# Kernel tuning notes

Measured on AMD Instinct MI355X. Metric: run time of the kernel, lower is better.

The kernel has to match this reference:

```python
import jax, jax.numpy as jnp
import numpy as np

B, P, ENC = 32, 196, 2048   # batch, num_pixels, encoder_dim
A, D, E = 512, 512, 512     # attention_dim, decoder_dim, embed_dim
V, L = 32000, 40            # vocab_size, caption length
T = L - 1                   # max decode steps (static)


def setup_inputs() -> dict:
    key = jax.random.key(0)
    ks = jax.random.split(key, 20)
    u = lambda k, shape, s=0.05: jax.random.uniform(k, shape, jnp.float32, -s, s)
    caplens = jax.random.randint(ks[2], (B,), 5, L + 1).at[0].set(L)
    return {
        "encoder_out": jax.random.normal(ks[0], (B, P, ENC), jnp.float32),
        "encoded_captions": jax.random.randint(ks[1], (B, L), 0, V),
        "caption_lengths": caplens,
        "embedding": u(ks[3], (V, E), 0.1),
        "W_enc": u(ks[4], (ENC, A)), "b_enc": jnp.zeros((A,), jnp.float32),
        "W_dec": u(ks[5], (D, A)),   "b_dec": jnp.zeros((A,), jnp.float32),
        "w_att": u(ks[6], (A, 1)),   "b_att": jnp.zeros((1,), jnp.float32),
        "W_ih": u(ks[7], (E + ENC, 4 * D)), "b_ih": jnp.zeros((4 * D,), jnp.float32),
        "W_hh": u(ks[8], (D, 4 * D)),       "b_hh": jnp.zeros((4 * D,), jnp.float32),
        "W_h": u(ks[9], (ENC, D)),  "b_h": jnp.zeros((D,), jnp.float32),
        "W_c": u(ks[10], (ENC, D)), "b_c": jnp.zeros((D,), jnp.float32),
        "W_fb": u(ks[11], (D, ENC)), "b_fb": jnp.zeros((ENC,), jnp.float32),
        "W_fc": u(ks[12], (D, V), 0.1), "b_fc": jnp.zeros((V,), jnp.float32),
    }


def reference(encoder_out, encoded_captions, caption_lengths, embedding,
              W_enc, b_enc, W_dec, b_dec, w_att, b_att,
              W_ih, b_ih, W_hh, b_hh, W_h, b_h, W_c, b_c,
              W_fb, b_fb, W_fc, b_fc):
    dec_len = caption_lengths - 1                       # [B]
    embs = embedding[encoded_captions]                  # [B, L, E]
    avg = encoder_out.mean(axis=1)                      # [B, ENC]
    h0 = avg @ W_h + b_h                                # [B, D]
    c0 = avg @ W_c + b_c
    enc_att = encoder_out @ W_enc + b_enc               # [B, P, A] (loop-invariant)

    xs = (jnp.transpose(embs[:, :T], (1, 0, 2)), jnp.arange(T))

    def step(carry, xt):
        h, c = carry
        emb_t, t = xt                                   # [B, E], scalar
        active = dec_len > t                            # [B] bool
        dec = h @ W_dec + b_dec                         # [B, A]
        e = (jax.nn.relu(enc_att + dec[:, None, :]) @ w_att)[..., 0] + b_att[0]  # [B, P]
        alpha = jax.nn.softmax(e, axis=1)               # [B, P]
        awe = jnp.einsum('bp,bpd->bd', alpha, encoder_out)
        gate = jax.nn.sigmoid(h @ W_fb + b_fb)          # [B, ENC]
        awe = gate * awe
        x = jnp.concatenate([emb_t, awe], axis=-1)      # [B, E+ENC]
        g = x @ W_ih + b_ih + h @ W_hh + b_hh           # [B, 4D]
        i_, f_, g_, o_ = jnp.split(g, 4, axis=-1)
        c_new = jax.nn.sigmoid(f_) * c + jax.nn.sigmoid(i_) * jnp.tanh(g_)
        h_new = jax.nn.sigmoid(o_) * jnp.tanh(c_new)
        preds = h_new @ W_fc + b_fc                     # [B, V]
        m = active[:, None].astype(h.dtype)
        h = jnp.where(active[:, None], h_new, h)        # only active rows advance
        c = jnp.where(active[:, None], c_new, c)
        return (h, c), (preds * m, alpha * m)

    (_, _), (preds, alphas) = jax.lax.scan(step, (h0, c0), xs)
    predictions = jnp.transpose(preds, (1, 0, 2))       # [B, T, V]
    alphas = jnp.transpose(alphas, (1, 0, 2))           # [B, T, P]
    return predictions, alphas
```

## Files before the change

### kernel.cpp

```cpp
#include <hip/hip_runtime.h>
#include <math.h>

#define NB 32
#define NP 196
#define ENC 2048
#define VOC 32000
#define LCAP 40
#define TS 39

typedef unsigned int uint_t;
typedef unsigned short ushort_t;

__device__ __forceinline__ float sigm(float x) { return 1.f / (1.f + expf(-x)); }

__device__ __forceinline__ ushort_t f2bf(float f) {
  uint_t u = __float_as_uint(f);
  u = (u + 0x7FFFu + ((u >> 16) & 1u)) >> 16;
  return (ushort_t)u;
}
__device__ __forceinline__ float bf2f(ushort_t s) { return __uint_as_float(((uint_t)s) << 16); }

typedef __attribute__((ext_vector_type(8))) short bf8v;
typedef __attribute__((ext_vector_type(16))) float f16v;
typedef __attribute__((ext_vector_type(4))) float f4v;

__device__ __forceinline__ f16v MFMA(bf8v a, bf8v b, f16v c) {
  return __builtin_amdgcn_mfma_f32_32x32x16_bf16(a, b, c, 0, 0, 0);
}

__device__ __forceinline__ void mfma_pipe_frag(
    const ushort_t* __restrict__ pa_h, const ushort_t* __restrict__ pa_l,
    const ushort_t* __restrict__ pb_h, const ushort_t* __restrict__ pb_l,
    int nquad, f16v& acc)
{
  bf8v ah0 = *(const bf8v*)(pa_h +    0), al0 = *(const bf8v*)(pa_l +    0);
  bf8v bh0 = *(const bf8v*)(pb_h +    0), bl0 = *(const bf8v*)(pb_l +    0);
  bf8v ah1 = *(const bf8v*)(pa_h +  512), al1 = *(const bf8v*)(pa_l +  512);
  bf8v bh1 = *(const bf8v*)(pb_h +  512), bl1 = *(const bf8v*)(pb_l +  512);
  bf8v ah2 = *(const bf8v*)(pa_h + 1024), al2 = *(const bf8v*)(pa_l + 1024);
  bf8v bh2 = *(const bf8v*)(pb_h + 1024), bl2 = *(const bf8v*)(pb_l + 1024);
  bf8v ah3 = *(const bf8v*)(pa_h + 1536), al3 = *(const bf8v*)(pa_l + 1536);
  bf8v bh3 = *(const bf8v*)(pb_h + 1536), bl3 = *(const bf8v*)(pb_l + 1536);
  for (int q = 0; q < nquad; ++q) {
    const size_t nk = (size_t)(q + 1) * 2048;
    const bool more = (q + 1 < nquad);
    acc = MFMA(ah0, bh0, acc); acc = MFMA(ah0, bl0, acc); acc = MFMA(al0, bh0, acc);
    if (more) {
      ah0 = *(const bf8v*)(pa_h + nk +    0); al0 = *(const bf8v*)(pa_l + nk +    0);
      bh0 = *(const bf8v*)(pb_h + nk +    0); bl0 = *(const bf8v*)(pb_l + nk +    0);
    }
    acc = MFMA(ah1, bh1, acc); acc = MFMA(ah1, bl1, acc); acc = MFMA(al1, bh1, acc);
    if (more) {
      ah1 = *(const bf8v*)(pa_h + nk +  512); al1 = *(const bf8v*)(pa_l + nk +  512);
      bh1 = *(const bf8v*)(pb_h + nk +  512); bl1 = *(const bf8v*)(pb_l + nk +  512);
    }
    acc = MFMA(ah2, bh2, acc); acc = MFMA(ah2, bl2, acc); acc = MFMA(al2, bh2, acc);
    if (more) {
      ah2 = *(const bf8v*)(pa_h + nk + 1024); al2 = *(const bf8v*)(pa_l + nk + 1024);
      bh2 = *(const bf8v*)(pb_h + nk + 1024); bl2 = *(const bf8v*)(pb_l + nk + 1024);
    }
    acc = MFMA(ah3, bh3, acc); acc = MFMA(ah3, bl3, acc); acc = MFMA(al3, bh3, acc);
    if (more) {
      ah3 = *(const bf8v*)(pa_h + nk + 1536); al3 = *(const bf8v*)(pa_l + nk + 1536);
      bh3 = *(const bf8v*)(pb_h + nk + 1536); bl3 = *(const bf8v*)(pb_l + nk + 1536);
    }
  }
}

__device__ __forceinline__ void mfma_pipe_fragAH(
    const ushort_t* __restrict__ pa_h,
    const ushort_t* __restrict__ pb_h, const ushort_t* __restrict__ pb_l,
    int nquad, f16v& acc)
{
  bf8v ah0 = *(const bf8v*)(pa_h +    0);
  bf8v bh0 = *(const bf8v*)(pb_h +    0), bl0 = *(const bf8v*)(pb_l +    0);
  bf8v ah1 = *(const bf8v*)(pa_h +  512);
  bf8v bh1 = *(const bf8v*)(pb_h +  512), bl1 = *(const bf8v*)(pb_l +  512);
  bf8v ah2 = *(const bf8v*)(pa_h + 1024);
  bf8v bh2 = *(const bf8v*)(pb_h + 1024), bl2 = *(const bf8v*)(pb_l + 1024);
  bf8v ah3 = *(const bf8v*)(pa_h + 1536);
  bf8v bh3 = *(const bf8v*)(pb_h + 1536), bl3 = *(const bf8v*)(pb_l + 1536);
  for (int q = 0; q < nquad; ++q) {
    const size_t nk = (size_t)(q + 1) * 2048;
    const bool more = (q + 1 < nquad);
    acc = MFMA(ah0, bh0, acc); acc = MFMA(ah0, bl0, acc);
    if (more) {
      ah0 = *(const bf8v*)(pa_h + nk +    0);
      bh0 = *(const bf8v*)(pb_h + nk +    0); bl0 = *(const bf8v*)(pb_l + nk +    0);
    }
    acc = MFMA(ah1, bh1, acc); acc = MFMA(ah1, bl1, acc);
    if (more) {
      ah1 = *(const bf8v*)(pa_h + nk +  512);
      bh1 = *(const bf8v*)(pb_h + nk +  512); bl1 = *(const bf8v*)(pb_l + nk +  512);
    }
    acc = MFMA(ah2, bh2, acc); acc = MFMA(ah2, bl2, acc);
    if (more) {
      ah2 = *(const bf8v*)(pa_h + nk + 1024);
      bh2 = *(const bf8v*)(pb_h + nk + 1024); bl2 = *(const bf8v*)(pb_l + nk + 1024);
    }
    acc = MFMA(ah3, bh3, acc); acc = MFMA(ah3, bl3, acc);
    if (more) {
      ah3 = *(const bf8v*)(pa_h + nk + 1536);
      bh3 = *(const bf8v*)(pb_h + nk + 1536); bl3 = *(const bf8v*)(pb_l + nk + 1536);
    }
  }
}

__device__ __forceinline__ void mfma_pipe_fragHH(
    const ushort_t* __restrict__ pa_h,
    const ushort_t* __restrict__ pb_h, int nquad, f16v& acc)
{
  bf8v ah0 = *(const bf8v*)(pa_h +    0);
  bf8v bh0 = *(const bf8v*)(pb_h +    0);
  bf8v ah1 = *(const bf8v*)(pa_h +  512);
  bf8v bh1 = *(const bf8v*)(pb_h +  512);
  bf8v ah2 = *(const bf8v*)(pa_h + 1024);
  bf8v bh2 = *(const bf8v*)(pb_h + 1024);
  bf8v ah3 = *(const bf8v*)(pa_h + 1536);
  bf8v bh3 = *(const bf8v*)(pb_h + 1536);
  for (int q = 0; q < nquad; ++q) {
    const size_t nk = (size_t)(q + 1) * 2048;
    const bool more = (q + 1 < nquad);
    acc = MFMA(ah0, bh0, acc);
    if (more) { ah0 = *(const bf8v*)(pa_h + nk +    0); bh0 = *(const bf8v*)(pb_h + nk +    0); }
    acc = MFMA(ah1, bh1, acc);
    if (more) { ah1 = *(const bf8v*)(pa_h + nk +  512); bh1 = *(const bf8v*)(pb_h + nk +  512); }
    acc = MFMA(ah2, bh2, acc);
    if (more) { ah2 = *(const bf8v*)(pa_h + nk + 1024); bh2 = *(const bf8v*)(pb_h + nk + 1024); }
    acc = MFMA(ah3, bh3, acc);
    if (more) { ah3 = *(const bf8v*)(pa_h + nk + 1536); bh3 = *(const bf8v*)(pb_h + nk + 1536); }
  }
}

#define CD_ROW(rr, g) (((rr) & 3) + 8 * ((rr) >> 2) + 4 * (g))

__global__ __launch_bounds__(256) void menc_att(
    const ushort_t* __restrict__ Ahi,
    const ushort_t* __restrict__ Whi, const ushort_t* __restrict__ Wlo,
    const float* __restrict__ benc, ushort_t* __restrict__ encatt_bf)
{
  __shared__ float tileS[4][32][33];
  int w = threadIdx.x >> 6, lane = threadIdx.x & 63;
  int mt = blockIdx.y;
  int ct = blockIdx.x * 4 + w;
  const ushort_t* pa_h = Ahi + ((size_t)mt * 128) * 512 + lane * 8;
  const ushort_t* pb_h = Whi + ((size_t)ct * 128) * 512 + lane * 8;
  const ushort_t* pb_l = Wlo + ((size_t)ct * 128) * 512 + lane * 8;
  f16v acc = (f16v)(0.0f);
  mfma_pipe_fragAH(pa_h, pb_h, pb_l, 32, acc);
  int r = lane & 31, g = lane >> 5;
  float bn = benc[ct * 32 + r];
#pragma unroll
  for (int rr = 0; rr < 16; ++rr)
    tileS[w][r][CD_ROW(rr, g)] = acc[rr] + bn;
  __syncthreads();
#pragma unroll
  for (int j = 0; j < 4; ++j) {
    int a_l = j * 8 + (lane >> 3);
    int p4 = (lane & 7) * 4;
    int n2 = ct * 32 + a_l;
#pragma unroll
    for (int jj = 0; jj < 4; ++jj) {
      int pl = p4 + jj;
      int rg = mt * 32 + pl;
      int b = rg / 196, pp = rg - b * 196;
      encatt_bf[((size_t)b * 512 + n2) * 196 + pp] = f2bf(tileS[w][a_l][pl]);
    }
  }
}

__global__ __launch_bounds__(256) void mk1(
    const ushort_t* __restrict__ hhi, const ushort_t* __restrict__ hlo,
    const ushort_t* __restrict__ W1hi, const ushort_t* __restrict__ W1lo,
    float* __restrict__ dec_gate)
{
  int w = threadIdx.x >> 6, lane = threadIdx.x & 63;
  int ct = blockIdx.x * 4 + w;
  const ushort_t* pa_h = hhi + lane * 8;
  const ushort_t* pa_l = hlo + lane * 8;
  const ushort_t* pb_h = W1hi + ((size_t)ct * 32) * 512 + lane * 8;
  const ushort_t* pb_l = W1lo + ((size_t)ct * 32) * 512 + lane * 8;
  f16v acc = (f16v)(0.0f);
  mfma_pipe_frag(pa_h, pa_l, pb_h, pb_l, 8, acc);
  int r = lane & 31, g = lane >> 5;
  int n = ct * 32 + r;
#pragma unroll
  for (int rr = 0; rr < 16; ++rr)
    dec_gate[CD_ROW(rr, g) * 2560 + n] = acc[rr];
}

__global__ __launch_bounds__(256) void mk3(
    const ushort_t* __restrict__ xhi, const ushort_t* __restrict__ xlo,
    const ushort_t* __restrict__ W3hi, const ushort_t* __restrict__ W3lo,
    float* __restrict__ P2)
{
  int w = threadIdx.x >> 6, lane = threadIdx.x & 63;
  int ct = blockIdx.x * 4 + w;
  int s = blockIdx.y;
  const ushort_t* pa_h = xhi + ((size_t)s * 20) * 512 + lane * 8;
  const ushort_t* pa_l = xlo + ((size_t)s * 20) * 512 + lane * 8;
  const ushort_t* pb_h = W3hi + ((size_t)ct * 160 + s * 20) * 512 + lane * 8;
  const ushort_t* pb_l = W3lo + ((size_t)ct * 160 + s * 20) * 512 + lane * 8;
  f16v acc = (f16v)(0.0f);
  mfma_pipe_frag(pa_h, pa_l, pb_h, pb_l, 5, acc);
  int r = lane & 31, g = lane >> 5;
  int n = ct * 32 + r;
#pragma unroll
  for (int rr = 0; rr < 16; ++rr)
    P2[(size_t)s * (32 * 2048) + CD_ROW(rr, g) * 2048 + n] = acc[rr];
}

__global__ __launch_bounds__(256) void mpreds(
    const ushort_t* __restrict__ hhist_hi,
    const ushort_t* __restrict__ Wfchi, const float* __restrict__ bfc,
    const int* __restrict__ clen, float* __restrict__ outp)
{
  int orig = blockIdx.x;
  int xcd = orig & 7, i = orig >> 3;
  int base = (xcd < 6) ? xcd * 1219 : 6 * 1219 + (xcd - 6) * 1218;
  int wgid = base + i;
  int ct4 = wgid / 39, mt = wgid - ct4 * 39;
  int w = threadIdx.x >> 6, lane = threadIdx.x & 63;
  int ct = ct4 * 4 + w;
  const ushort_t* pa_h = hhist_hi + ((size_t)mt * 32) * 512 + lane * 8;
  const ushort_t* pb_h = Wfchi + ((size_t)ct * 32) * 512 + lane * 8;
  f16v acc = (f16v)(0.0f);
  mfma_pipe_fragHH(pa_h, pb_h, 8, acc);
  int r = lane & 31, g = lane >> 5;
  int n = ct * 32 + r;
  float bn = bfc[n];
#pragma unroll
  for (int rr = 0; rr < 16; ++rr) {
    int b = CD_ROW(rr, g);
    bool act = clen[b] - 1 > mt;
    outp[(size_t)b * (TS * VOC) + (size_t)mt * VOC + n] = act ? (acc[rr] + bn) : 0.f;
  }
}

__global__ __launch_bounds__(256) void convAe_fused(
    const float* __restrict__ src, ushort_t* __restrict__ dhi,
    ushort_t* __restrict__ enc_bf)
{
  int mt = blockIdx.x;
  int kc = blockIdx.y * 4 + (threadIdx.x >> 6);
  int l = threadIdx.x & 63;
  int r = l & 31, g = l >> 5;
  size_t si = (size_t)(mt * 32 + r) * 2048 + kc * 16 + g * 8;
  const float* s = src + si;
  float4 v0 = *(const float4*)s, v1 = *(const float4*)(s + 4);
  ushort4 h0, h1;
  h0.x = f2bf(v0.x); h0.y = f2bf(v0.y); h0.z = f2bf(v0.z); h0.w = f2bf(v0.w);
  h1.x = f2bf(v1.x); h1.y = f2bf(v1.y); h1.z = f2bf(v1.z); h1.w = f2bf(v1.w);
  size_t off = ((size_t)mt * 128 + kc) * 512 + (size_t)l * 8;
  *(ushort4*)&dhi[off] = h0; *(ushort4*)&dhi[off + 4] = h1;
  *(ushort4*)&enc_bf[si] = h0; *(ushort4*)&enc_bf[si + 4] = h1;
}

__global__ __launch_bounds__(256) void convA_emb_frag(
    const float* __restrict__ Emb, const int* __restrict__ caps,
    ushort_t* __restrict__ dhi, ushort_t* __restrict__ dlo)
{
  int mt = blockIdx.x;
  int kc = blockIdx.y * 4 + (threadIdx.x >> 6);
  int l = threadIdx.x & 63;
  int r = l & 31, g = l >> 5;
  int tok = caps[r * LCAP + mt];
  const float* s = Emb + (size_t)tok * 512 + kc * 16 + g * 8;
  float4 v0 = *(const float4*)s, v1 = *(const float4*)(s + 4);
  ushort4 h0, l0, h1, l1;
  h0.x = f2bf(v0.x); l0.x = f2bf(v0.x - bf2f(h0.x));
  h0.y = f2bf(v0.y); l0.y = f2bf(v0.y - bf2f(h0.y));
  h0.z = f2bf(v0.z); l0.z = f2bf(v0.z - bf2f(h0.z));
  h0.w = f2bf(v0.w); l0.w = f2bf(v0.w - bf2f(h0.w));
  h1.x = f2bf(v1.x); l1.x = f2bf(v1.x - bf2f(h1.x));
  h1.y = f2bf(v1.y); l1.y = f2bf(v1.y - bf2f(h1.y));
  h1.z = f2bf(v1.z); l1.z = f2bf(v1.z - bf2f(h1.z));
  h1.w = f2bf(v1.w); l1.w = f2bf(v1.w - bf2f(h1.w));
  size_t off = ((size_t)mt * 32 + kc) * 512 + (size_t)l * 8;
  *(ushort4*)&dhi[off] = h0; *(ushort4*)&dhi[off + 4] = h1;
  *(ushort4*)&dlo[off] = l0; *(ushort4*)&dlo[off + 4] = l1;
}

__global__ __launch_bounds__(256) void convT_frag(
    const float* __restrict__ src, int N,
    ushort_t* __restrict__ dhi, ushort_t* __restrict__ dlo,
    int nkc_dst, int kc_off)
{
  int ct = blockIdx.x;
  int kc = blockIdx.y * 4 + (threadIdx.x >> 6);
  int l = threadIdx.x & 63;
  int c = l & 31, g = l >> 5;
  const float* s = src + (size_t)(kc * 16 + g * 8) * N + ct * 32 + c;
  ushort_t hi8[8], lo8[8];
#pragma unroll
  for (int e = 0; e < 8; ++e) {
    float f = s[(size_t)e * N];
    hi8[e] = f2bf(f); lo8[e] = f2bf(f - bf2f(hi8[e]));
  }
  size_t off = ((size_t)ct * nkc_dst + kc_off + kc) * 512 + (size_t)l * 8;
  *(ushort4*)&dhi[off]     = make_ushort4(hi8[0], hi8[1], hi8[2], hi8[3]);
  *(ushort4*)&dhi[off + 4] = make_ushort4(hi8[4], hi8[5], hi8[6], hi8[7]);
  *(ushort4*)&dlo[off]     = make_ushort4(lo8[0], lo8[1], lo8[2], lo8[3]);
  *(ushort4*)&dlo[off + 4] = make_ushort4(lo8[4], lo8[5], lo8[6], lo8[7]);
}

__global__ __launch_bounds__(256) void convT_fragH(
    const float* __restrict__ src, int N,
    ushort_t* __restrict__ dhi, int nkc_dst, int kc_off)
{
  int ct = blockIdx.x;
  int kc = blockIdx.y * 4 + (threadIdx.x >> 6);
  int l = threadIdx.x & 63;
  int c = l & 31, g = l >> 5;
  const float* s = src + (size_t)(kc * 16 + g * 8) * N + ct * 32 + c;
  ushort_t hi8[8];
#pragma unroll
  for (int e = 0; e < 8; ++e) hi8[e] = f2bf(s[(size_t)e * N]);
  size_t off = ((size_t)ct * nkc_dst + kc_off + kc) * 512 + (size_t)l * 8;
  *(ushort4*)&dhi[off]     = make_ushort4(hi8[0], hi8[1], hi8[2], hi8[3]);
  *(ushort4*)&dhi[off + 4] = make_ushort4(hi8[4], hi8[5], hi8[6], hi8[7]);
}

__global__ __launch_bounds__(256) void mavg_frag(
    const float* __restrict__ enc, ushort_t* __restrict__ dhi, ushort_t* __restrict__ dlo)
{
  int b = blockIdx.x;
  int e = blockIdx.y * 256 + threadIdx.x;
  float s = 0.f;
  const float* base = enc + (size_t)b * 196 * 2048 + e;
  for (int p = 0; p < NP; ++p) s += base[(size_t)p * 2048];
  s *= (1.f / 196.f);
  ushort_t hi = f2bf(s), lo = f2bf(s - bf2f(hi));
  size_t off = (size_t)(e >> 4) * 512 + ((e >> 3) & 1) * 256 + b * 8 + (e & 7);
  dhi[off] = hi; dlo[off] = lo;
}

__global__ __launch_bounds__(256) void mh0c0(
    const ushort_t* __restrict__ avg_hi, const ushort_t* __restrict__ avg_lo,
    const ushort_t* __restrict__ Whc_hi, const ushort_t* __restrict__ Whc_lo,
    const float* __restrict__ b_h, const float* __restrict__ b_c,
    float* __restrict__ h0f, float* __restrict__ cbuf)
{
  int w = threadIdx.x >> 6, lane = threadIdx.x & 63;
  int ct = blockIdx.x * 4 + w;
  const ushort_t* pa_h = avg_hi + lane * 8;
  const ushort_t* pa_l = avg_lo + lane * 8;
  const ushort_t* pb_h = Whc_hi + ((size_t)ct * 128) * 512 + lane * 8;
  const ushort_t* pb_l = Whc_lo + ((size_t)ct * 128) * 512 + lane * 8;
  f16v acc = (f16v)(0.0f);
  mfma_pipe_frag(pa_h, pa_l, pb_h, pb_l, 32, acc);
  int r = lane & 31, g = lane >> 5;
  int n = ct * 32 + r;
  if (ct < 16) {
    float bn = b_h[n];
#pragma unroll
    for (int rr = 0; rr < 16; ++rr)
      h0f[CD_ROW(rr, g) * 512 + n] = acc[rr] + bn;
  } else {
    int n2 = n - 512;
    float bn = b_c[n2];
#pragma unroll
    for (int rr = 0; rr < 16; ++rr)
      cbuf[CD_ROW(rr, g) * 512 + n2] = acc[rr] + bn;
  }
}

__global__ __launch_bounds__(256) void m_emb(
    const ushort_t* __restrict__ eFhi, const ushort_t* __restrict__ eFlo,
    const ushort_t* __restrict__ Whi, const ushort_t* __restrict__ Wlo,
    const float* __restrict__ b1, const float* __restrict__ b2,
    float* __restrict__ embproj)
{
  int w = threadIdx.x >> 6, lane = threadIdx.x & 63;
  int mt = blockIdx.y;
  int ct = blockIdx.x * 4 + w;
  const ushort_t* pa_h = eFhi + ((size_t)mt * 32) * 512 + lane * 8;
  const ushort_t* pa_l = eFlo + ((size_t)mt * 32) * 512 + lane * 8;
  const ushort_t* pb_h = Whi + ((size_t)ct * 32) * 512 + lane * 8;
  const ushort_t* pb_l = Wlo + ((size_t)ct * 32) * 512 + lane * 8;
  f16v acc = (f16v)(0.0f);
  mfma_pipe_frag(pa_h, pa_l, pb_h, pb_l, 8, acc);
  int r = lane & 31, g = lane >> 5;
  int n = ct * 32 + r;
  float bn = b1[n] + b2[n];
#pragma unroll
  for (int rr = 0; rr < 16; ++rr)
    embproj[(size_t)(mt * 32 + CD_ROW(rr, g)) * 2048 + n] = acc[rr] + bn;
}

__global__ __launch_bounds__(256) void hsplit_frag(
    const float* __restrict__ h0f,
    ushort_t* __restrict__ hhi, ushort_t* __restrict__ hlo,
    ushort_t* __restrict__ xhi, ushort_t* __restrict__ xlo)
{
  int idx = blockIdx.x * 256 + threadIdx.x;
  int b = idx >> 6, dq = idx & 63, d0 = dq << 3;
  ushort4 h0v, h1v, l0v, l1v;
  ushort_t hh[8], hl[8];
#pragma unroll
  for (int j = 0; j < 8; ++j) {
    float v = h0f[b * 512 + d0 + j];
    hh[j] = f2bf(v); hl[j] = f2bf(v - bf2f(hh[j]));
  }
  h0v = make_ushort4(hh[0], hh[1], hh[2], hh[3]); h1v = make_ushort4(hh[4], hh[5], hh[6], hh[7]);
  l0v = make_ushort4(hl[0], hl[1], hl[2], hl[3]); l1v = make_ushort4(hl[4], hl[5], hl[6], hl[7]);
  int kc = d0 >> 4, g = (d0 >> 3) & 1;
  size_t off = ((size_t)kc * 64 + g * 32 + b) * 8;
  *(ushort4*)&hhi[off] = h0v; *(ushort4*)&hhi[off + 4] = h1v;
  *(ushort4*)&hlo[off] = l0v; *(ushort4*)&hlo[off + 4] = l1v;
  int xk0 = 2048 + d0;
  size_t offx = ((size_t)(xk0 >> 4) * 64 + g * 32 + b) * 8;
  *(ushort4*)&xhi[offx] = h0v; *(ushort4*)&xhi[offx + 4] = h1v;
  *(ushort4*)&xlo[offx] = l0v; *(ushort4*)&xlo[offx + 4] = l1v;
}

__global__ __launch_bounds__(512) void k2ab(
    const float* __restrict__ dec_gate, const float* __restrict__ bdec,
    const float* __restrict__ bfb, const float* __restrict__ watt,
    const float* __restrict__ batt, const ushort_t* __restrict__ encatt_bf,
    const ushort_t* __restrict__ enc_bf, const int* __restrict__ clen,
    float* __restrict__ outa, ushort_t* __restrict__ xhi, ushort_t* __restrict__ xlo,
    int t)
{
  int b = blockIdx.x, yh = blockIdx.y, tid = threadIdx.x;
  __shared__ float dec_s[512], watt_s[512], part_s[2][256], red_s[256], al_s[196];
  __shared__ float aw_s[2][256][4];
  dec_s[tid] = dec_gate[b * 2560 + tid] + bdec[tid];
  watt_s[tid] = watt[tid];
  __syncthreads();
  int p = tid & 255, half = tid >> 8;
  float acc = 0.f;
  if (p < NP) {
    const ushort_t* col = encatt_bf + (size_t)b * 512 * 196 + p;
    int a0 = half * 256;
#pragma unroll 8
    for (int a = a0; a < a0 + 256; ++a)
      acc += fmaxf(bf2f(col[(size_t)a * 196]) + dec_s[a], 0.f) * watt_s[a];
  }
  part_s[half][p] = acc;
  __syncthreads();
  float e = -1e30f;
  if (tid < NP) e = part_s[0][tid] + part_s[1][tid] + batt[0];
  if (tid < 256) red_s[tid] = e;
  __syncthreads();
  for (int wd = 128; wd > 0; wd >>= 1) {
    if (tid < wd) red_s[tid] = fmaxf(red_s[tid], red_s[tid + wd]);
    __syncthreads();
  }
  float m = red_s[0];
  __syncthreads();
  float ex = (tid < NP) ? expf(e - m) : 0.f;
  if (tid < 256) red_s[tid] = ex;
  __syncthreads();
  for (int wd = 128; wd > 0; wd >>= 1) {
    if (tid < wd) red_s[tid] += red_s[tid + wd];
    __syncthreads();
  }
  float inv = 1.f / red_s[0];
  if (tid < NP) {
    float al = ex * inv;
    al_s[tid] = al;
    if (yh == 0) {
      bool act = clen[b] - 1 > t;
      outa[(size_t)(b * TS + t) * NP + tid] = act ? al : 0.f;
    }
  }
  __syncthreads();
  int q = tid & 255, sp = tid >> 8;
  int d = yh * 1024 + q * 4;
  float ax = 0.f, ay = 0.f, az = 0.f, aw = 0.f;
  int p0 = sp * 98;
#pragma unroll 7
  for (int pp = p0; pp < p0 + 98; ++pp) {
    float al = al_s[pp];
    ushort4 ev = *(const ushort4*)&enc_bf[(size_t)(b * NP + pp) * ENC + d];
    ax += al * bf2f(ev.x); ay += al * bf2f(ev.y);
    az += al * bf2f(ev.z); aw += al * bf2f(ev.w);
  }
  aw_s[sp][q][0] = ax; aw_s[sp][q][1] = ay; aw_s[sp][q][2] = az; aw_s[sp][q][3] = aw;
  __syncthreads();
  if (sp == 0) {
    ax += aw_s[1][q][0]; ay += aw_s[1][q][1];
    az += aw_s[1][q][2]; aw += aw_s[1][q][3];
    float4 gg = *(const float4*)&dec_gate[b * 2560 + 512 + d];
    float4 bb = *(const float4*)&bfb[d];
    float v0 = sigm(gg.x + bb.x) * ax;
    float v1 = sigm(gg.y + bb.y) * ay;
    float v2 = sigm(gg.z + bb.z) * az;
    float v3 = sigm(gg.w + bb.w) * aw;
    ushort4 hi, lo;
    hi.x = f2bf(v0); lo.x = f2bf(v0 - bf2f(hi.x));
    hi.y = f2bf(v1); lo.y = f2bf(v1 - bf2f(hi.y));
    hi.z = f2bf(v2); lo.z = f2bf(v2 - bf2f(hi.z));
    hi.w = f2bf(v3); lo.w = f2bf(v3 - bf2f(hi.w));
    size_t off = ((size_t)(d >> 4) * 64 + ((d >> 3) & 1) * 32 + b) * 8 + (d & 7);
    *(ushort4*)&xhi[off] = hi;
    *(ushort4*)&xlo[off] = lo;
  }
}

__global__ __launch_bounds__(64) void k4_lstm_frag(
    const float* __restrict__ P2, const float* __restrict__ embproj,
    const int* __restrict__ clen, float* __restrict__ c,
    ushort_t* __restrict__ hhi, ushort_t* __restrict__ hlo,
    ushort_t* __restrict__ xhi, ushort_t* __restrict__ xlo,
    ushort_t* __restrict__ hhist_hi, int t)
{
  int idx = blockIdx.x * 64 + threadIdx.x;
  int b = idx >> 6, dq = idx & 63, d0 = dq << 3;
  bool act = clen[b] - 1 > t;
  const float* ep = embproj + (size_t)(t * 32 + b) * 2048;
  f4v i0 = *(const f4v*)&ep[d0],        i1 = *(const f4v*)&ep[d0 + 4];
  f4v f0 = *(const f4v*)&ep[512 + d0],  f1 = *(const f4v*)&ep[512 + d0 + 4];
  f4v g0 = *(const f4v*)&ep[1024 + d0], g1 = *(const f4v*)&ep[1024 + d0 + 4];
  f4v o0 = *(const f4v*)&ep[1536 + d0], o1 = *(const f4v*)&ep[1536 + d0 + 4];
#pragma unroll
  for (int s = 0; s < 8; ++s) {
    const float* p2 = P2 + (size_t)s * 65536 + b * 2048;
    i0 += *(const f4v*)&p2[d0];        i1 += *(const f4v*)&p2[d0 + 4];
    f0 += *(const f4v*)&p2[512 + d0];  f1 += *(const f4v*)&p2[512 + d0 + 4];
    g0 += *(const f4v*)&p2[1024 + d0]; g1 += *(const f4v*)&p2[1024 + d0 + 4];
    o0 += *(const f4v*)&p2[1536 + d0]; o1 += *(const f4v*)&p2[1536 + d0 + 4];
  }
  f4v c0 = *(const f4v*)&c[b * 512 + d0], c1 = *(const f4v*)&c[b * 512 + d0 + 4];
  ushort_t hh[8], hl[8];
  f4v cn0, cn1;
#pragma unroll
  for (int j = 0; j < 8; ++j) {
    float iv = j < 4 ? i0[j] : i1[j - 4];
    float fv = j < 4 ? f0[j] : f1[j - 4];
    float gv = j < 4 ? g0[j] : g1[j - 4];
    float ov = j < 4 ? o0[j] : o1[j - 4];
    float cv = j < 4 ? c0[j] : c1[j - 4];
    float cn = sigm(fv) * cv + sigm(iv) * tanhf(gv);
    float hn = sigm(ov) * tanhf(cn);
    if (j < 4) cn0[j] = cn; else cn1[j - 4] = cn;
    hh[j] = f2bf(hn); hl[j] = f2bf(hn - bf2f(hh[j]));
  }
  ushort4 h0v = make_ushort4(hh[0], hh[1], hh[2], hh[3]);
  ushort4 h1v = make_ushort4(hh[4], hh[5], hh[6], hh[7]);
  ushort4 l0v = make_ushort4(hl[0], hl[1], hl[2], hl[3]);
  ushort4 l1v = make_ushort4(hl[4], hl[5], hl[6], hl[7]);
  int kc = d0 >> 4, g = (d0 >> 3) & 1;
  size_t offh = ((size_t)(t * 32 + kc)) * 512 + ((size_t)g * 32 + b) * 8;
  *(ushort4*)&hhist_hi[offh] = h0v; *(ushort4*)&hhist_hi[offh + 4] = h1v;
  if (!act) return;
  *(f4v*)&c[b * 512 + d0] = cn0; *(f4v*)&c[b * 512 + d0 + 4] = cn1;
  size_t off = ((size_t)kc * 64 + g * 32 + b) * 8;
  *(ushort4*)&hhi[off] = h0v; *(ushort4*)&hhi[off + 4] = h1v;
  *(ushort4*)&hlo[off] = l0v; *(ushort4*)&hlo[off + 4] = l1v;
  int xk0 = 2048 + d0;
  size_t offx = ((size_t)(xk0 >> 4) * 64 + g * 32 + b) * 8;
  *(ushort4*)&xhi[offx] = h0v; *(ushort4*)&xhi[offx + 4] = h1v;
  *(ushort4*)&xlo[offx] = l0v; *(ushort4*)&xlo[offx + 4] = l1v;
}

extern "C" void kernel_launch(void* const* d_in, const int* in_sizes, int n_in,
                              void* d_out, int out_size, void* d_ws, size_t ws_size,
                              hipStream_t stream)
{
  (void)in_sizes; (void)n_in; (void)out_size; (void)ws_size;
  const float* enc   = (const float*)d_in[0];
  const int*   caps  = (const int*)d_in[1];
  const int*   clen  = (const int*)d_in[2];
  const float* emb   = (const float*)d_in[3];
  const float* W_enc = (const float*)d_in[4];
  const float* b_enc = (const float*)d_in[5];
  const float* W_dec = (const float*)d_in[6];
  const float* b_dec = (const float*)d_in[7];
  const float* w_att = (const float*)d_in[8];
  const float* b_att = (const float*)d_in[9];
  const float* W_ih  = (const float*)d_in[10];
  const float* b_ih  = (const float*)d_in[11];
  const float* W_hh  = (const float*)d_in[12];
  const float* b_hh  = (const float*)d_in[13];
  const float* W_h   = (const float*)d_in[14];
  const float* b_h   = (const float*)d_in[15];
  const float* W_c   = (const float*)d_in[16];
  const float* b_c   = (const float*)d_in[17];
  const float* W_fb  = (const float*)d_in[18];
  const float* b_fb  = (const float*)d_in[19];
  const float* W_fc  = (const float*)d_in[20];
  const float* b_fc  = (const float*)d_in[21];

  float* out_preds = (float*)d_out;
  float* out_alpha = out_preds + (size_t)NB * TS * VOC;

  char* p = (char*)d_ws;
  ushort_t* encatt_bf = (ushort_t*)p;     p += 12845056;
  float* embproj  = (float*)p;            p += 10223616;
  float* P2buf    = (float*)p;            p += 2097152;
  float* dec_gate = (float*)p;            p += 327680;
  ushort_t* x_lo  = (ushort_t*)p;         p += 262144;
  float* h0f      = (float*)p;            p += 65536;
  float* cbuf     = (float*)p;            p += 65536;
  float* al_ws    = (float*)p;            p += 25088;
  ushort_t* h_hi  = (ushort_t*)p;         p += 32768;
  ushort_t* h_lo  = (ushort_t*)p;         p += 32768;
  ushort_t* x_hi  = (ushort_t*)p;         p += 163840;
  p += 262144 - 25088 - 32768 - 32768 - 163840;
  ushort_t* e_hi  = (ushort_t*)p;         p += 25690112;
  ushort_t* enc_bf = (ushort_t*)p;        p += 25690112;
  ushort_t* We_hi = (ushort_t*)p;         p += 2097152;
  ushort_t* We_lo = (ushort_t*)p;         p += 2097152;
  ushort_t* W1_hi = (ushort_t*)p;         p += 2621440;
  ushort_t* W1_lo = (ushort_t*)p;         p += 2621440;
  ushort_t* W3_hi = (ushort_t*)p;         p += 10485760;
  ushort_t* W3_lo = (ushort_t*)p;         p += 10485760;
  ushort_t* Wf_hi = (ushort_t*)p;         p += 32768000;
  ushort_t* WiE_hi = (ushort_t*)p;        p += 2097152;
  ushort_t* WiE_lo = (ushort_t*)p;        p += 2097152;
  ushort_t* eF_hi  = (ushort_t*)p;        p += 1277952;
  ushort_t* eF_lo  = (ushort_t*)p;        p += 1277952;
  ushort_t* hh_hi  = (ushort_t*)p;        p += 1277952;
  (void)al_ws;

  ushort_t* avg_hi = (ushort_t*)embproj;
  ushort_t* avg_lo = avg_hi + 65536;
  ushort_t* Whc_hi = Wf_hi;
  ushort_t* Whc_lo = Wf_hi + 2097152;

  mavg_frag<<<dim3(32, 8), 256, 0, stream>>>(enc, avg_hi, avg_lo);
  convT_frag<<<dim3(16, 32), 256, 0, stream>>>(W_h, 512, Whc_hi, Whc_lo, 128, 0);
  convT_frag<<<dim3(16, 32), 256, 0, stream>>>(W_c, 512,
      Whc_hi + (size_t)16 * 128 * 512, Whc_lo + (size_t)16 * 128 * 512, 128, 0);
  mh0c0<<<dim3(8), 256, 0, stream>>>(avg_hi, avg_lo, Whc_hi, Whc_lo, b_h, b_c, h0f, cbuf);
  convAe_fused<<<dim3(196, 32), 256, 0, stream>>>(enc, e_hi, enc_bf);
  convT_frag<<<dim3(16, 32), 256, 0, stream>>>(W_enc, 512, We_hi, We_lo, 128, 0);
  convT_frag<<<dim3(16, 8), 256, 0, stream>>>(W_dec, 512, W1_hi, W1_lo, 32, 0);
  convT_frag<<<dim3(64, 8), 256, 0, stream>>>(W_fb, 2048,
      W1_hi + (size_t)16 * 32 * 512, W1_lo + (size_t)16 * 32 * 512, 32, 0);
  convT_frag<<<dim3(64, 32), 256, 0, stream>>>(W_ih + (size_t)512 * 2048, 2048,
      W3_hi, W3_lo, 160, 0);
  convT_frag<<<dim3(64, 8), 256, 0, stream>>>(W_hh, 2048, W3_hi, W3_lo, 160, 128);
  convT_fragH<<<dim3(1000, 8), 256, 0, stream>>>(W_fc, VOC, Wf_hi, 32, 0);
  convA_emb_frag<<<dim3(39, 8), 256, 0, stream>>>(emb, caps, eF_hi, eF_lo);
  convT_frag<<<dim3(64, 8), 256, 0, stream>>>(W_ih, 2048, WiE_hi, WiE_lo, 32, 0);

  menc_att<<<dim3(4, 196), 256, 0, stream>>>(e_hi, We_hi, We_lo, b_enc, encatt_bf);
  m_emb<<<dim3(16, 39), 256, 0, stream>>>(eF_hi, eF_lo, WiE_hi, WiE_lo, b_ih, b_hh, embproj);
  hsplit_frag<<<dim3(8), 256, 0, stream>>>(h0f, h_hi, h_lo, x_hi, x_lo);
  mk1<<<dim3(20), 256, 0, stream>>>(h_hi, h_lo, W1_hi, W1_lo, dec_gate);

  for (int t = 0; t < TS; ++t) {
    k2ab<<<dim3(32, 2), 512, 0, stream>>>(dec_gate, b_dec, b_fb, w_att, b_att,
                                          encatt_bf, enc_bf, clen, out_alpha,
                                          x_hi, x_lo, t);
    mk3<<<dim3(16, 8), 256, 0, stream>>>(x_hi, x_lo, W3_hi, W3_lo, P2buf);
    k4_lstm_frag<<<dim3(32), 64, 0, stream>>>(P2buf, embproj, clen, cbuf,
                                              h_hi, h_lo, x_hi, x_lo, hh_hi, t);
    if (t < TS - 1)
      mk1<<<dim3(20), 256, 0, stream>>>(h_hi, h_lo, W1_hi, W1_lo, dec_gate);
  }

  mpreds<<<dim3(9750), 256, 0, stream>>>(hh_hi, Wf_hi, b_fc, clen, out_preds);
}
```

Measured before the change: 2.075 ms.

## Fuse LSTM cell update with decoder/gate projection; halve mk3 split-K

Merges the LSTM elementwise kernel and the following h-projection GEMM (mk1) into one kernel, k41. Each of its 20 blocks recomputes the full LSTM cell update redundantly and stages the new h (hi/lo bf16) in shared memory for its MFMA tile. Only block 0 writes the state back to global memory. Split-K in mk3 drops from 8 to 4 slices, each twice as long, which halves the partial sums k41 has to reduce. Together these remove one launch per timestep, but the cell update is now repeated 20 times and mk3 runs fewer blocks with a longer serial K loop.

```diff
diff --git a/kernel.cpp b/kernel.cpp
--- a/kernel.cpp
+++ b/kernel.cpp
@@ -197,17 +197,111 @@
   int w = threadIdx.x >> 6, lane = threadIdx.x & 63;
   int ct = blockIdx.x * 4 + w;
   int s = blockIdx.y;
-  const ushort_t* pa_h = xhi + ((size_t)s * 20) * 512 + lane * 8;
-  const ushort_t* pa_l = xlo + ((size_t)s * 20) * 512 + lane * 8;
-  const ushort_t* pb_h = W3hi + ((size_t)ct * 160 + s * 20) * 512 + lane * 8;
-  const ushort_t* pb_l = W3lo + ((size_t)ct * 160 + s * 20) * 512 + lane * 8;
+  const ushort_t* pa_h = xhi + ((size_t)s * 40) * 512 + lane * 8;
+  const ushort_t* pa_l = xlo + ((size_t)s * 40) * 512 + lane * 8;
+  const ushort_t* pb_h = W3hi + ((size_t)ct * 160 + s * 40) * 512 + lane * 8;
+  const ushort_t* pb_l = W3lo + ((size_t)ct * 160 + s * 40) * 512 + lane * 8;
   f16v acc = (f16v)(0.0f);
-  mfma_pipe_frag(pa_h, pa_l, pb_h, pb_l, 5, acc);
+  mfma_pipe_frag(pa_h, pa_l, pb_h, pb_l, 10, acc);
   int r = lane & 31, g = lane >> 5;
   int n = ct * 32 + r;
 #pragma unroll
   for (int rr = 0; rr < 16; ++rr)
     P2[(size_t)s * (32 * 2048) + CD_ROW(rr, g) * 2048 + n] = acc[rr];
+}
+
+__global__ __launch_bounds__(256) void k41(
+    const float* __restrict__ P2, const float* __restrict__ embproj,
+    const int* __restrict__ clen, float* __restrict__ c,
+    ushort_t* __restrict__ hhi, ushort_t* __restrict__ hlo,
+    ushort_t* __restrict__ xhi, ushort_t* __restrict__ xlo,
+    ushort_t* __restrict__ hhist_hi,
+    const ushort_t* __restrict__ W1hi, const ushort_t* __restrict__ W1lo,
+    float* __restrict__ dec_gate, int t, int do_k1)
+{
+  __shared__ ushort_t hLh[16384];
+  __shared__ ushort_t hLl[16384];
+  int bid = blockIdx.x, tid = threadIdx.x;
+#pragma unroll 2
+  for (int it = 0; it < 8; ++it) {
+    int idx = it * 256 + tid;
+    int b = idx >> 6, dq = idx & 63, d0 = dq << 3;
+    bool act = clen[b] - 1 > t;
+    const float* ep = embproj + (size_t)(t * 32 + b) * 2048;
+    f4v i0 = *(const f4v*)&ep[d0],        i1 = *(const f4v*)&ep[d0 + 4];
+    f4v f0 = *(const f4v*)&ep[512 + d0],  f1 = *(const f4v*)&ep[512 + d0 + 4];
+    f4v g0 = *(const f4v*)&ep[1024 + d0], g1 = *(const f4v*)&ep[1024 + d0 + 4];
+    f4v o0 = *(const f4v*)&ep[1536 + d0], o1 = *(const f4v*)&ep[1536 + d0 + 4];
+#pragma unroll
+    for (int s = 0; s < 4; ++s) {
+      const float* p2 = P2 + (size_t)s * 65536 + b * 2048;
+      i0 += *(const f4v*)&p2[d0];        i1 += *(const f4v*)&p2[d0 + 4];
+      f0 += *(const f4v*)&p2[512 + d0];  f1 += *(const f4v*)&p2[512 + d0 + 4];
+      g0 += *(const f4v*)&p2[1024 + d0]; g1 += *(const f4v*)&p2[1024 + d0 + 4];
+      o0 += *(const f4v*)&p2[1536 + d0]; o1 += *(const f4v*)&p2[1536 + d0 + 4];
+    }
+    f4v c0 = *(const f4v*)&c[b * 512 + d0], c1 = *(const f4v*)&c[b * 512 + d0 + 4];
+    ushort_t hh[8], hl[8];
+    f4v cn0, cn1;
+#pragma unroll
+    for (int j = 0; j < 8; ++j) {
+      float iv = j < 4 ? i0[j] : i1[j - 4];
+      float fv = j < 4 ? f0[j] : f1[j - 4];
+      float gv = j < 4 ? g0[j] : g1[j - 4];
+      float ov = j < 4 ? o0[j] : o1[j - 4];
+      float cv = j < 4 ? c0[j] : c1[j - 4];
+      float cn = sigm(fv) * cv + sigm(iv) * tanhf(gv);
+      float hn = sigm(ov) * tanhf(cn);
+      if (j < 4) cn0[j] = cn; else cn1[j - 4] = cn;
+      hh[j] = f2bf(hn); hl[j] = f2bf(hn - bf2f(hh[j]));
+    }
+    ushort4 h0v = make_ushort4(hh[0], hh[1], hh[2], hh[3]);
+    ushort4 h1v = make_ushort4(hh[4], hh[5], hh[6], hh[7]);
+    ushort4 l0v = make_ushort4(hl[0], hl[1], hl[2], hl[3]);
+    ushort4 l1v = make_ushort4(hl[4], hl[5], hl[6], hl[7]);
+    int kc = d0 >> 4, g = (d0 >> 3) & 1;
+    size_t off = ((size_t)kc * 64 + g * 32 + b) * 8;
+    ushort4 sh0 = h0v, sh1 = h1v, sl0 = l0v, sl1 = l1v;
+    if (!act) {
+      sh0 = *(const ushort4*)&hhi[off]; sh1 = *(const ushort4*)&hhi[off + 4];
+      sl0 = *(const ushort4*)&hlo[off]; sl1 = *(const ushort4*)&hlo[off + 4];
+    }
+    *(ushort4*)&hLh[off] = sh0; *(ushort4*)&hLh[off + 4] = sh1;
+    *(ushort4*)&hLl[off] = sl0; *(ushort4*)&hLl[off + 4] = sl1;
+    if (bid == 0) {
+      size_t offh = ((size_t)(t * 32 + kc)) * 512 + ((size_t)g * 32 + b) * 8;
+      *(ushort4*)&hhist_hi[offh] = h0v; *(ushort4*)&hhist_hi[offh + 4] = h1v;
+      if (act) {
+        *(f4v*)&c[b * 512 + d0] = cn0; *(f4v*)&c[b * 512 + d0 + 4] = cn1;
+        *(ushort4*)&hhi[off] = h0v; *(ushort4*)&hhi[off + 4] = h1v;
+        *(ushort4*)&hlo[off] = l0v; *(ushort4*)&hlo[off + 4] = l1v;
+        int xk0 = 2048 + d0;
+        size_t offx = ((size_t)(xk0 >> 4) * 64 + g * 32 + b) * 8;
+        *(ushort4*)&xhi[offx] = h0v; *(ushort4*)&xhi[offx + 4] = h1v;
+        *(ushort4*)&xlo[offx] = l0v; *(ushort4*)&xlo[offx + 4] = l1v;
+      }
+    }
+  }
+  __syncthreads();
+  if (!do_k1) return;
+  int w = tid >> 6, lane = tid & 63;
+  int r = lane & 31, g2 = lane >> 5;
+  int ct = bid * 4 + w;
+  const ushort_t* pbh = W1hi + ((size_t)ct * 32) * 512 + lane * 8;
+  const ushort_t* pbl = W1lo + ((size_t)ct * 32) * 512 + lane * 8;
+  f16v acc = (f16v)(0.0f);
+#pragma unroll 4
+  for (int q = 0; q < 32; ++q) {
+    bf8v a_h = *(const bf8v*)&hLh[lane * 8 + q * 512];
+    bf8v a_l = *(const bf8v*)&hLl[lane * 8 + q * 512];
+    bf8v b_h = *(const bf8v*)(pbh + q * 512);
+    bf8v b_l = *(const bf8v*)(pbl + q * 512);
+    acc = MFMA(a_h, b_h, acc); acc = MFMA(a_h, b_l, acc); acc = MFMA(a_l, b_h, acc);
+  }
+  int n = ct * 32 + r;
+#pragma unroll
+  for (int rr = 0; rr < 16; ++rr)
+    dec_gate[CD_ROW(rr, g2) * 2560 + n] = acc[rr];
 }
 
 __global__ __launch_bounds__(256) void mpreds(
@@ -497,62 +591,6 @@
     *(ushort4*)&xhi[off] = hi;
     *(ushort4*)&xlo[off] = lo;
   }
-}
-
-__global__ __launch_bounds__(64) void k4_lstm_frag(
-    const float* __restrict__ P2, const float* __restrict__ embproj,
-    const int* __restrict__ clen, float* __restrict__ c,
-    ushort_t* __restrict__ hhi, ushort_t* __restrict__ hlo,
-    ushort_t* __restrict__ xhi, ushort_t* __restrict__ xlo,
-    ushort_t* __restrict__ hhist_hi, int t)
-{
-  int idx = blockIdx.x * 64 + threadIdx.x;
-  int b = idx >> 6, dq = idx & 63, d0 = dq << 3;
-  bool act = clen[b] - 1 > t;
-  const float* ep = embproj + (size_t)(t * 32 + b) * 2048;
-  f4v i0 = *(const f4v*)&ep[d0],        i1 = *(const f4v*)&ep[d0 + 4];
-  f4v f0 = *(const f4v*)&ep[512 + d0],  f1 = *(const f4v*)&ep[512 + d0 + 4];
-  f4v g0 = *(const f4v*)&ep[1024 + d0], g1 = *(const f4v*)&ep[1024 + d0 + 4];
-  f4v o0 = *(const f4v*)&ep[1536 + d0], o1 = *(const f4v*)&ep[1536 + d0 + 4];
-#pragma unroll
-  for (int s = 0; s < 8; ++s) {
-    const float* p2 = P2 + (size_t)s * 65536 + b * 2048;
-    i0 += *(const f4v*)&p2[d0];        i1 += *(const f4v*)&p2[d0 + 4];
-    f0 += *(const f4v*)&p2[512 + d0];  f1 += *(const f4v*)&p2[512 + d0 + 4];
-    g0 += *(const f4v*)&p2[1024 + d0]; g1 += *(const f4v*)&p2[1024 + d0 + 4];
-    o0 += *(const f4v*)&p2[1536 + d0]; o1 += *(const f4v*)&p2[1536 + d0 + 4];
-  }
-  f4v c0 = *(const f4v*)&c[b * 512 + d0], c1 = *(const f4v*)&c[b * 512 + d0 + 4];
-  ushort_t hh[8], hl[8];
-  f4v cn0, cn1;
-#pragma unroll
-  for (int j = 0; j < 8; ++j) {
-    float iv = j < 4 ? i0[j] : i1[j - 4];
-    float fv = j < 4 ? f0[j] : f1[j - 4];
-    float gv = j < 4 ? g0[j] : g1[j - 4];
-    float ov = j < 4 ? o0[j] : o1[j - 4];
-    float cv = j < 4 ? c0[j] : c1[j - 4];
-    float cn = sigm(fv) * cv + sigm(iv) * tanhf(gv);
-    float hn = sigm(ov) * tanhf(cn);
-    if (j < 4) cn0[j] = cn; else cn1[j - 4] = cn;
-    hh[j] = f2bf(hn); hl[j] = f2bf(hn - bf2f(hh[j]));
-  }
-  ushort4 h0v = make_ushort4(hh[0], hh[1], hh[2], hh[3]);
-  ushort4 h1v = make_ushort4(hh[4], hh[5], hh[6], hh[7]);
-  ushort4 l0v = make_ushort4(hl[0], hl[1], hl[2], hl[3]);
-  ushort4 l1v = make_ushort4(hl[4], hl[5], hl[6], hl[7]);
-  int kc = d0 >> 4, g = (d0 >> 3) & 1;
-  size_t offh = ((size_t)(t * 32 + kc)) * 512 + ((size_t)g * 32 + b) * 8;
-  *(ushort4*)&hhist_hi[offh] = h0v; *(ushort4*)&hhist_hi[offh + 4] = h1v;
-  if (!act) return;
-  *(f4v*)&c[b * 512 + d0] = cn0; *(f4v*)&c[b * 512 + d0 + 4] = cn1;
-  size_t off = ((size_t)kc * 64 + g * 32 + b) * 8;
-  *(ushort4*)&hhi[off] = h0v; *(ushort4*)&hhi[off + 4] = h1v;
-  *(ushort4*)&hlo[off] = l0v; *(ushort4*)&hlo[off + 4] = l1v;
-  int xk0 = 2048 + d0;
-  size_t offx = ((size_t)(xk0 >> 4) * 64 + g * 32 + b) * 8;
-  *(ushort4*)&xhi[offx] = h0v; *(ushort4*)&xhi[offx + 4] = h1v;
-  *(ushort4*)&xlo[offx] = l0v; *(ushort4*)&xlo[offx + 4] = l1v;
 }
 
 extern "C" void kernel_launch(void* const* d_in, const int* in_sizes, int n_in,
@@ -646,11 +684,10 @@
     k2ab<<<dim3(32, 2), 512, 0, stream>>>(dec_gate, b_dec, b_fb, w_att, b_att,
                                           encatt_bf, enc_bf, clen, out_alpha,
                                           x_hi, x_lo, t);
-    mk3<<<dim3(16, 8), 256, 0, stream>>>(x_hi, x_lo, W3_hi, W3_lo, P2buf);
-    k4_lstm_frag<<<dim3(32), 64, 0, stream>>>(P2buf, embproj, clen, cbuf,
-                                              h_hi, h_lo, x_hi, x_lo, hh_hi, t);
-    if (t < TS - 1)
-      mk1<<<dim3(20), 256, 0, stream>>>(h_hi, h_lo, W1_hi, W1_lo, dec_gate);
+    mk3<<<dim3(16, 4), 256, 0, stream>>>(x_hi, x_lo, W3_hi, W3_lo, P2buf);
+    k41<<<dim3(20), 256, 0, stream>>>(P2buf, embproj, clen, cbuf,
+                                      h_hi, h_lo, x_hi, x_lo, hh_hi,
+                                      W1_hi, W1_lo, dec_gate, t, (t < TS - 1) ? 1 : 0);
   }
 
   mpreds<<<dim3(9750), 256, 0, stream>>>(hh_hi, Wf_hi, b_fc, clen, out_preds);
```

Result: slower. 3.044 ms (+46.7%).
